# Optimization experiments

Hardware: AMD Instinct MI355X
Metric: run time of the kernel (lower is better)

## Reference

```python
import jax, jax.numpy as jnp
import numpy as np

K = 16          # max_points
S = 3           # num_scales
DM = 256        # d_model
KD = 16         # k_dim geometric projection
TAU = 1e-4
LN_EPS = 1e-5


def _boundaries():
    edges = [(i, j) for i in range(K) for j in range(i + 1, K)]
    tris = [(i, j, k) for i in range(K) for j in range(i + 1, K) for k in range(j + 1, K)]
    E, T = len(edges), len(tris)
    B1 = np.zeros((K, E), np.float32)
    for e, (i, j) in enumerate(edges):
        B1[i, e] = -1.0
        B1[j, e] = 1.0
    eidx = {e: n for n, e in enumerate(edges)}
    B2 = np.zeros((E, T), np.float32)
    for t, (i, j, k) in enumerate(tris):
        B2[eidx[(j, k)], t] = 1.0
        B2[eidx[(i, k)], t] = -1.0
        B2[eidx[(i, j)], t] = 1.0
    ei = np.array([e[0] for e in edges])
    ej = np.array([e[1] for e in edges])
    tij = np.array([eidx[(a, b)] for a, b, c in tris])
    tjk = np.array([eidx[(b, c)] for a, b, c in tris])
    tik = np.array([eidx[(a, c)] for a, b, c in tris])
    return (jnp.asarray(B1), jnp.asarray(B2), jnp.asarray(np.abs(B1)),
            jnp.asarray(ei), jnp.asarray(ej), jnp.asarray(tij), jnp.asarray(tjk), jnp.asarray(tik))

_B1, _B2, _ABS, _EI, _EJ, _TIJ, _TJK, _TIK = _boundaries()
E = _B1.shape[1]  # 120


def _ln(x, g, b):
    m = jnp.mean(x, -1, keepdims=True)
    v = jnp.mean((x - m) ** 2, -1, keepdims=True)
    return (x - m) * jax.lax.rsqrt(v + LN_EPS) * g + b


def setup_inputs() -> dict:
    key = jax.random.key(0)
    ks = jax.random.split(key, 12)
    B = 1024
    p = lambda k, *sh: 0.02 * jax.random.normal(k, sh, dtype=jnp.float32)
    return {
        'x': jax.random.normal(ks[0], (B, K, DM), dtype=jnp.float32),
        'mask': jnp.ones((B, K), dtype=jnp.float32),
        'Wg': p(ks[1], DM, KD), 'bg': jnp.zeros((KD,), jnp.float32),
        'log_scales': jnp.linspace(-1.5, 1.5, S, dtype=jnp.float32),
        'Wv': p(ks[2], DM, DM * S), 'bv': jnp.zeros((DM * S,), jnp.float32),
        'We': p(ks[3], DM, DM * S), 'be': jnp.zeros((DM * S,), jnp.float32),
        'Wo': p(ks[4], DM * S * 2, DM), 'bo': jnp.zeros((DM,), jnp.float32),
        'ln1_g': jnp.ones((DM,), jnp.float32), 'ln1_b': jnp.zeros((DM,), jnp.float32),
        'ln2_g': jnp.ones((DM,), jnp.float32), 'ln2_b': jnp.zeros((DM,), jnp.float32),
        'Wf1': p(ks[5], DM, DM * 4), 'bf1': jnp.zeros((DM * 4,), jnp.float32),
        'Wf2': p(ks[6], DM * 4, DM), 'bf2': jnp.zeros((DM,), jnp.float32),
    }


def reference(x, mask, Wg, bg, log_scales, Wv, bv, We, be, Wo, bo,
              ln1_g, ln1_b, ln2_g, ln2_b, Wf1, bf1, Wf2, bf2):
    B = x.shape[0]
    xn = _ln(x, ln1_g, ln1_b)
    P = xn @ Wg + bg                                   # [B,K,KD]
    m2 = mask[:, :, None] * mask[:, None, :]           # [B,K,K]
    p2 = jnp.sum(P * P, -1)
    Dsq = jnp.maximum(p2[:, :, None] + p2[:, None, :] - 2.0 * jnp.einsum('bkc,blc->bkl', P, P), 0.0) * m2
    sig2 = jnp.exp(log_scales) ** 2                    # [S]
    V0 = (xn @ Wv + bv).reshape(B, K, S, DM).transpose(0, 2, 1, 3)   # [B,S,K,D]
    Eraw = jnp.einsum('ke,bkd->bed', _ABS, xn)         # [B,E,D]
    Ein = (Eraw @ We + be).reshape(B, E, S, DM).transpose(0, 2, 1, 3)  # [B,S,E,D]
    aff = jnp.exp(-Dsq[:, None] / (2.0 * sig2[None, :, None, None] + 1e-8)) * m2[:, None]  # [B,S,K,K]
    W1 = aff[:, :, _EI, _EJ]                           # [B,S,E]
    W2 = W1[:, :, _TIJ] * W1[:, :, _TJK] * W1[:, :, _TIK]  # [B,S,T]
    L0 = jnp.einsum('ke,bse,le->bskl', _B1, W1, _B1) + TAU * jnp.eye(K, dtype=x.dtype)
    node_upd = jnp.einsum('bskl,bsld->bskd', L0, V0)
    term_down = jnp.einsum('ke,bk,kf->bef', _B1, mask, _B1)
    term_up = jnp.einsum('et,bst,ft->bsef', _B2, W2, _B2)
    L1 = term_down[:, None] + term_up + TAU * jnp.eye(E, dtype=x.dtype)
    edge_msg = jnp.einsum('bsef,bsfd->bsed', L1, Ein)
    edge_upd = jnp.einsum('ke,bsed->bskd', _ABS, edge_msg)
    nu = node_upd.transpose(0, 2, 1, 3).reshape(B, K, S * DM)
    eu = edge_upd.transpose(0, 2, 1, 3).reshape(B, K, S * DM)
    x = x + (jnp.concatenate([nu, eu], -1) @ Wo + bo)  # residual + attn_out (dropout=eval noop)
    h = _ln(x, ln2_g, ln2_b)
    return x + (jax.nn.gelu(h @ Wf1 + bf1, approximate=False) @ Wf2 + bf2)
```

## Files before the change

kernel.cpp:

```cpp
#include <hip/hip_runtime.h>
#include <hip/hip_bf16.h>
#include <cstdint>
#include <cstddef>

#define TAU 1e-4f
#define LN_EPS 1e-5f

typedef unsigned short ushort_t;
typedef unsigned int uint_t;
typedef __attribute__((ext_vector_type(8))) short short8;
typedef __attribute__((ext_vector_type(4))) float f32x4;

__device__ __forceinline__ ushort_t f2bf(float f) {
    union { float f; unsigned int u; } c; c.f = f;
    unsigned int r = (c.u + 0x7fffu + ((c.u >> 16) & 1u)) >> 16;
    return (ushort_t)r;
}
__device__ __forceinline__ void glds16(const void* g, void* l) {
    __builtin_amdgcn_global_load_lds((const __attribute__((address_space(1))) unsigned int*)g,
                                     (__attribute__((address_space(3))) unsigned int*)l,
                                     16, 0, 0);
}

__global__ __launch_bounds__(256) void kA(
    const float* __restrict__ xg, const float* __restrict__ maskg,
    const float* __restrict__ Wg, const float* __restrict__ bg,
    const float* __restrict__ ls, const float* __restrict__ g1,
    const float* __restrict__ b1, ushort_t* __restrict__ Mcat,
    float* __restrict__ gbuf,
    const float* __restrict__ Wv, const float* __restrict__ We,
    const float* __restrict__ Wo, const float* __restrict__ bv,
    const float* __restrict__ be, const float* __restrict__ Wf1,
    const float* __restrict__ Wf2, ushort_t* __restrict__ WcatT,
    ushort_t* __restrict__ Wf1T, ushort_t* __restrict__ Wf2T,
    float* __restrict__ cvpart, float* __restrict__ beWo) {
    __shared__ __align__(16) float POOL[7968];
    const int tid = threadIdx.x;

    if (blockIdx.x >= 1024) {
        const int id = blockIdx.x - 1024;
        if (id < 384) {
            float (*rowS)[256] = (float(*)[256])POOL;
            const int q0 = (id & 63) * 4;
            const int w = id >> 6;
            const int half = w / 3, s = w - half * 3;
            const float* src = half ? We : Wv;
#pragma unroll
            for (int r = 0; r < 4; ++r)
                rowS[r][tid] = src[(size_t)(q0 + r) * 768 + s * 256 + tid];
            __syncthreads();
            const float* wo = Wo + (size_t)(half * 768 + s * 256) * 256 + tid;
            float a0 = 0.f, a1 = 0.f, a2 = 0.f, a3 = 0.f;
            for (int d = 0; d < 256; ++d) {
                float wv = wo[(size_t)d * 256];
                a0 += rowS[0][d] * wv; a1 += rowS[1][d] * wv;
                a2 += rowS[2][d] * wv; a3 += rowS[3][d] * wv;
            }
            const int rt = half * 3 + s;
            ushort4 pk;
            pk.x = f2bf(a0); pk.y = f2bf(a1); pk.z = f2bf(a2); pk.w = f2bf(a3);
            *(ushort4*)&WcatT[(size_t)tid * 1536 + rt * 256 + q0] = pk;
        } else if (id < 390) {
            const int w = id - 384;
            const int half = w / 3, s = w - half * 3;
            const float* vec = half ? be : bv;
            POOL[tid] = vec[s * 256 + tid];
            __syncthreads();
            const float* wo = Wo + (size_t)(half * 768 + s * 256) * 256 + tid;
            float acc = 0.f;
            for (int d = 0; d < 256; ++d) acc += POOL[d] * wo[(size_t)d * 256];
            if (half) beWo[s * 256 + tid] = acc;
            else cvpart[s * 256 + tid] = acc;
        } else {
            float (*tS)[65] = (float(*)[65])POOL;
            const float* src; ushort_t* dst;
            int sr0, sc0, ss, dr0, dc0, ds_;
            if (id < 454) {
                int t = id - 390; int ki = t & 3, ni = t >> 2;
                src = Wf1; ss = 1024; sr0 = ki * 64; sc0 = ni * 64;
                dst = Wf1T; ds_ = 256; dr0 = ni * 64; dc0 = ki * 64;
            } else {
                int t = id - 454; int ki = t >> 2, ni = t & 3;
                src = Wf2; ss = 256; sr0 = ki * 64; sc0 = ni * 64;
                dst = Wf2T; ds_ = 1024; dr0 = ni * 64; dc0 = ki * 64;
            }
            const int rl = tid >> 6, cl = tid & 63;
#pragma unroll
            for (int p = 0; p < 16; ++p) {
                int r = p * 4 + rl;
                tS[r][cl] = src[(size_t)(sr0 + r) * ss + sc0 + cl];
            }
            __syncthreads();
#pragma unroll
            for (int p = 0; p < 16; ++p) {
                int r = p * 4 + rl;
                dst[(size_t)(dr0 + r) * ds_ + dc0 + cl] = f2bf(tS[cl][r]);
            }
        }
        return;
    }

    const int b = blockIdx.x;
    float (*XS)[260] = (float(*)[260])POOL;
    float (*WgTh)[132] = (float(*)[132])(POOL + 4160);
    float* Ms = POOL + 4160;
    float (*Wh)[16][17] = (float(*)[16][17])(POOL + 6272);
    float* Ts = POOL + 7088;
    float (*Pl)[17] = (float(*)[17])(POOL + 7136);
    float (*dotm)[17] = (float(*)[17])(POOL + 7408);
    float (*DsqS)[17] = (float(*)[17])(POOL + 7680);
    float* mk = POOL + 7952;

    const float* xb = xg + (size_t)b * 4096;
#pragma unroll
    for (int i = 0; i < 4; ++i) {
        int idx = tid * 4 + i * 1024;
        int k = idx >> 8, c = idx & 255;
        float4 v = *(const float4*)&xb[idx];
        XS[k][c] = v.x; XS[k][c + 1] = v.y; XS[k][c + 2] = v.z; XS[k][c + 3] = v.w;
    }
    if (tid < 16) mk[tid] = maskg[b * 16 + tid];
    __syncthreads();

    {
        const int k = tid >> 4, c = tid & 15;
        float s = 0.f;
#pragma unroll
        for (int j = 0; j < 16; ++j) s += XS[k][c + 16 * j];
        for (int off = 8; off; off >>= 1) s += __shfl_down(s, off, 16);
        float mean = __shfl(s, 0, 16) * (1.f / 256.f);
        float vs = 0.f;
#pragma unroll
        for (int j = 0; j < 16; ++j) { float d = XS[k][c + 16 * j] - mean; vs += d * d; }
        for (int off = 8; off; off >>= 1) vs += __shfl_down(vs, off, 16);
        float rstd = rsqrtf(__shfl(vs, 0, 16) * (1.f / 256.f) + LN_EPS);
#pragma unroll
        for (int j = 0; j < 16; ++j) {
            int cc = c + 16 * j;
            XS[k][cc] = (XS[k][cc] - mean) * rstd * g1[cc] + b1[cc];
        }
    }
    __syncthreads();

    {
        const int k = tid >> 4, c = tid & 15;
        const int ql = tid >> 1, hf = tid & 1;
        float acc = bg[c];
        {
            const float4* wp = (const float4*)(Wg + ql * 16 + hf * 8);
            float4 w0 = wp[0], w1 = wp[1];
            WgTh[hf * 8 + 0][ql] = w0.x; WgTh[hf * 8 + 1][ql] = w0.y;
            WgTh[hf * 8 + 2][ql] = w0.z; WgTh[hf * 8 + 3][ql] = w0.w;
            WgTh[hf * 8 + 4][ql] = w1.x; WgTh[hf * 8 + 5][ql] = w1.y;
            WgTh[hf * 8 + 6][ql] = w1.z; WgTh[hf * 8 + 7][ql] = w1.w;
        }
        __syncthreads();
        const float4* wp2 = (const float4*)(Wg + (128 + ql) * 16 + hf * 8);
        float4 w20 = wp2[0], w21 = wp2[1];
#pragma unroll
        for (int q4 = 0; q4 < 32; ++q4) {
            float4 wv = *(const float4*)&WgTh[c][q4 * 4];
            float4 xv = *(const float4*)&XS[k][q4 * 4];
            acc += wv.x * xv.x + wv.y * xv.y + wv.z * xv.z + wv.w * xv.w;
        }
        __syncthreads();
        WgTh[hf * 8 + 0][ql] = w20.x; WgTh[hf * 8 + 1][ql] = w20.y;
        WgTh[hf * 8 + 2][ql] = w20.z; WgTh[hf * 8 + 3][ql] = w20.w;
        WgTh[hf * 8 + 4][ql] = w21.x; WgTh[hf * 8 + 5][ql] = w21.y;
        WgTh[hf * 8 + 6][ql] = w21.z; WgTh[hf * 8 + 7][ql] = w21.w;
        __syncthreads();
#pragma unroll
        for (int q4 = 0; q4 < 32; ++q4) {
            float4 wv = *(const float4*)&WgTh[c][q4 * 4];
            float4 xv = *(const float4*)&XS[k][128 + q4 * 4];
            acc += wv.x * xv.x + wv.y * xv.y + wv.z * xv.z + wv.w * xv.w;
        }
        Pl[k][c] = acc;
    }
    __syncthreads();
    const int k = tid >> 4, m = tid & 15;
    {
        float d = 0.f;
#pragma unroll
        for (int c = 0; c < 16; ++c) d += Pl[k][c] * Pl[m][c];
        dotm[k][m] = d;
    }
    __syncthreads();
    {
        float v = dotm[k][k] + dotm[m][m] - 2.f * dotm[k][m];
        DsqS[k][m] = fmaxf(v, 0.f) * mk[k] * mk[m];
    }
    {
        float d = DsqS[k][m];
        float mm = mk[k] * mk[m];
#pragma unroll
        for (int s = 0; s < 3; ++s) {
            float i2 = 1.f / (2.f * expf(2.f * ls[s]) + 1e-8f);
            Wh[s][k][m] = (k == m) ? 0.f : expf(-d * i2) * mm;
        }
    }
    __syncthreads();
    if (tid < 48) {
        int s = tid >> 4, j = tid & 15;
        float t = 0.f;
        for (int i = 0; i < j; ++i) {
            float d = 0.f;
            for (int jj = j + 1; jj < 16; ++jj) d += Wh[s][j][jj] * Wh[s][i][jj];
            t += Wh[s][i][j] * d;
        }
        Ts[s * 16 + j] = t;
    }
    __syncthreads();
    float gd = 0.f;
#pragma unroll
    for (int o = 0; o < 16; ++o) {
        if (o == m) continue;
        int u = o < m ? o : m, v = o < m ? m : o;
        float gu = (u == k) ? (float)(2 * k - 15) : ((u > k) ? 1.f : -1.f);
        float gv = (v == k) ? (float)(2 * k - 15) : ((v > k) ? 1.f : -1.f);
        gd += -gu * mk[u] + gv * mk[v];
        if (u == k || v == k) gd += TAU;
    }
#pragma unroll
    for (int s = 0; s < 3; ++s) {
        float rs = 0.f;
#pragma unroll
        for (int o = 0; o < 16; ++o) rs += Wh[s][k][o];
        float l0 = (k == m) ? (rs + TAU) : -Wh[s][k][m];
        float G = gd + ((k == m) ? 4.f * Ts[s * 16 + k] : 0.f);
        Ms[s * 256 + tid] = l0;
        Ms[768 + s * 256 + tid] = G;
        float gg = G;
        for (int off = 8; off; off >>= 1) gg += __shfl_down(gg, off, 16);
        if (m == 0) gbuf[b * 48 + k * 3 + s] = 0.5f * gg;
    }
    __syncthreads();

    {
        const int q2 = (tid & 127) * 2;
        const int rtbase = (tid >> 7) * 3;
        float xv0[16], xv1[16];
#pragma unroll
        for (int l = 0; l < 16; ++l) { xv0[l] = XS[l][q2]; xv1[l] = XS[l][q2 + 1]; }
        const size_t obase = (size_t)b * 16 * 1536;
#pragma unroll
        for (int rtt = 0; rtt < 3; ++rtt) {
            const int rt = rtbase + rtt;
#pragma unroll
            for (int kk = 0; kk < 16; ++kk) {
                const float4* mp = (const float4*)&Ms[rt * 256 + kk * 16];
                float4 m0 = mp[0], m1 = mp[1], m2 = mp[2], m3 = mp[3];
                float a0 = m0.x * xv0[0] + m0.y * xv0[1] + m0.z * xv0[2] + m0.w * xv0[3]
                         + m1.x * xv0[4] + m1.y * xv0[5] + m1.z * xv0[6] + m1.w * xv0[7]
                         + m2.x * xv0[8] + m2.y * xv0[9] + m2.z * xv0[10] + m2.w * xv0[11]
                         + m3.x * xv0[12] + m3.y * xv0[13] + m3.z * xv0[14] + m3.w * xv0[15];
                float a1 = m0.x * xv1[0] + m0.y * xv1[1] + m0.z * xv1[2] + m0.w * xv1[3]
                         + m1.x * xv1[4] + m1.y * xv1[5] + m1.z * xv1[6] + m1.w * xv1[7]
                         + m2.x * xv1[8] + m2.y * xv1[9] + m2.z * xv1[10] + m2.w * xv1[11]
                         + m3.x * xv1[12] + m3.y * xv1[13] + m3.z * xv1[14] + m3.w * xv1[15];
                uint_t pk = (uint_t)f2bf(a0) | ((uint_t)f2bf(a1) << 16);
                *(uint_t*)&Mcat[obase + (size_t)kk * 1536 + rt * 256 + q2] = pk;
            }
        }
    }
}

__device__ __forceinline__ void gemm64_db(
    const ushort_t* __restrict__ A, const ushort_t* __restrict__ Bt,
    int Kdim, int m0, int n0, f32x4 acc[2][4],
    ushort_t (*As0)[32], ushort_t (*As1)[32],
    ushort_t (*Bs0)[32], ushort_t (*Bs1)[32]) {
    const int tid = threadIdx.x;
    const int wave = tid >> 6, lane = tid & 63;
    const int lq = lane >> 4, lr = lane & 15;
    const int wm = wave >> 1, wn = wave & 1;
    const int r = tid >> 2, ca = (tid & 3) << 3;
    const ushort_t* Ag  = A  + (size_t)(m0 + r) * Kdim + ca;
    const ushort_t* Bg0 = Bt + (size_t)(n0 + r) * Kdim + ca;
    const ushort_t* Bg1 = Bt + (size_t)(n0 + 64 + r) * Kdim + ca;
    char* aD0  = (char*)As0 + wave * 1024;
    char* aD1  = (char*)As1 + wave * 1024;
    char* b0D0 = (char*)Bs0 + wave * 1024;
    char* b0D1 = (char*)Bs0 + 4096 + wave * 1024;
    char* b1D0 = (char*)Bs1 + wave * 1024;
    char* b1D1 = (char*)Bs1 + 4096 + wave * 1024;

    glds16(Ag, aD0); glds16(Bg0, b0D0); glds16(Bg1, b0D1);

    for (int kt = 0; kt < Kdim; kt += 64) {
        {
            const int kn = kt + 32;
            if (kn < Kdim) {
                glds16(Ag + kn, aD1); glds16(Bg0 + kn, b1D0); glds16(Bg1 + kn, b1D1);
                asm volatile("s_waitcnt vmcnt(3)" ::: "memory");
            } else {
                asm volatile("s_waitcnt vmcnt(0)" ::: "memory");
            }
            __builtin_amdgcn_s_barrier();
            short8 af[2], bfr[4];
#pragma unroll
            for (int i = 0; i < 2; ++i) af[i] = *(const short8*)&As0[wm * 32 + i * 16 + lr][lq * 8];
#pragma unroll
            for (int j = 0; j < 4; ++j) bfr[j] = *(const short8*)&Bs0[wn * 64 + j * 16 + lr][lq * 8];
#pragma unroll
            for (int i = 0; i < 2; ++i)
#pragma unroll
                for (int j = 0; j < 4; ++j)
                    acc[i][j] = __builtin_amdgcn_mfma_f32_16x16x32_bf16(af[i], bfr[j], acc[i][j], 0, 0, 0);
            asm volatile("s_waitcnt lgkmcnt(0)" ::: "memory");
            __builtin_amdgcn_s_barrier();
        }
        {
            const int kn = kt + 64;
            if (kn < Kdim) {
                glds16(Ag + kn, aD0); glds16(Bg0 + kn, b0D0); glds16(Bg1 + kn, b0D1);
                asm volatile("s_waitcnt vmcnt(3)" ::: "memory");
            } else {
                asm volatile("s_waitcnt vmcnt(0)" ::: "memory");
            }
            __builtin_amdgcn_s_barrier();
            short8 af[2], bfr[4];
#pragma unroll
            for (int i = 0; i < 2; ++i) af[i] = *(const short8*)&As1[wm * 32 + i * 16 + lr][lq * 8];
#pragma unroll
            for (int j = 0; j < 4; ++j) bfr[j] = *(const short8*)&Bs1[wn * 64 + j * 16 + lr][lq * 8];
#pragma unroll
            for (int i = 0; i < 2; ++i)
#pragma unroll
                for (int j = 0; j < 4; ++j)
                    acc[i][j] = __builtin_amdgcn_mfma_f32_16x16x32_bf16(af[i], bfr[j], acc[i][j], 0, 0, 0);
            asm volatile("s_waitcnt lgkmcnt(0)" ::: "memory");
            __builtin_amdgcn_s_barrier();
        }
    }
}

__global__ __launch_bounds__(256) void kZY_gemm(
    const ushort_t* __restrict__ Mcat, const ushort_t* __restrict__ WcatT,
    const float* __restrict__ xin, const float* __restrict__ bo,
    const float* __restrict__ cvpart, const float* __restrict__ beWo,
    const float* __restrict__ gbuf, float* __restrict__ xp) {
    __shared__ ushort_t As0[64][32], As1[64][32];
    __shared__ ushort_t Bs0[128][32], Bs1[128][32];
    __shared__ float cvS[128], bewS[3][128], gblk[64][3];
    const int tid = threadIdx.x;
    const int m0 = blockIdx.x * 64, n0 = blockIdx.y * 128;
    if (tid < 128) {
        int n = n0 + tid;
        cvS[tid] = bo[n] + TAU * (cvpart[n] + cvpart[256 + n] + cvpart[512 + n]);
        bewS[0][tid] = beWo[n];
        bewS[1][tid] = beWo[256 + n];
        bewS[2][tid] = beWo[512 + n];
    }
    if (tid < 192) { int rr = tid / 3, s = tid - rr * 3; gblk[rr][s] = gbuf[(size_t)(m0 + rr) * 3 + s]; }
    f32x4 acc[2][4] = {};
    gemm64_db(Mcat, WcatT, 1536, m0, n0, acc, As0, As1, Bs0, Bs1);
    const int wave = tid >> 6, lane = tid & 63, lq = lane >> 4, lr = lane & 15;
    const int wm = wave >> 1, wn = wave & 1;
#pragma unroll
    for (int i = 0; i < 2; ++i)
#pragma unroll
        for (int j = 0; j < 4; ++j) {
            int nl = wn * 64 + j * 16 + lr;
#pragma unroll
            for (int v = 0; v < 4; ++v) {
                int rl = wm * 32 + i * 16 + lq * 4 + v;
                size_t idx = (size_t)(m0 + rl) * 256 + n0 + nl;
                xp[idx] = acc[i][j][v] + xin[idx] + cvS[nl] +
                          gblk[rl][0] * bewS[0][nl] + gblk[rl][1] * bewS[1][nl] +
                          gblk[rl][2] * bewS[2][nl];
            }
        }
}

__global__ __launch_bounds__(256) void k_ln2(const float* __restrict__ xp,
                                             const float* __restrict__ g2,
                                             const float* __restrict__ b2,
                                             ushort_t* __restrict__ h) {
    const int tid = threadIdx.x;
    const int row = blockIdx.x * 4 + (tid >> 6);
    const int lane = tid & 63;
    const float* xr = xp + (size_t)row * 256;
    float v0 = xr[lane], v1 = xr[lane + 64], v2 = xr[lane + 128], v3 = xr[lane + 192];
    float s = v0 + v1 + v2 + v3;
    for (int m = 32; m; m >>= 1) s += __shfl_xor(s, m, 64);
    float mean = s * (1.f / 256.f);
    float d0 = v0 - mean, d1 = v1 - mean, d2 = v2 - mean, d3 = v3 - mean;
    float q = d0 * d0 + d1 * d1 + d2 * d2 + d3 * d3;
    for (int m = 32; m; m >>= 1) q += __shfl_xor(q, m, 64);
    float rstd = rsqrtf(q * (1.f / 256.f) + LN_EPS);
    ushort_t* hr = h + (size_t)row * 256;
    hr[lane] = f2bf(d0 * rstd * g2[lane] + b2[lane]);
    hr[lane + 64] = f2bf(d1 * rstd * g2[lane + 64] + b2[lane + 64]);
    hr[lane + 128] = f2bf(d2 * rstd * g2[lane + 128] + b2[lane + 128]);
    hr[lane + 192] = f2bf(d3 * rstd * g2[lane + 192] + b2[lane + 192]);
}

__global__ __launch_bounds__(256) void k3_gemm(const ushort_t* __restrict__ h,
                                               const ushort_t* __restrict__ Wf1T,
                                               const float* __restrict__ bf1,
                                               ushort_t* __restrict__ F1g) {
    __shared__ ushort_t As0[64][32], As1[64][32];
    __shared__ ushort_t Bs0[128][32], Bs1[128][32];
    const int tid = threadIdx.x;
    const int m0 = blockIdx.x * 64, n0 = blockIdx.y * 128;
    f32x4 acc[2][4] = {};
    gemm64_db(h, Wf1T, 256, m0, n0, acc, As0, As1, Bs0, Bs1);
    const int wave = tid >> 6, lane = tid & 63, lq = lane >> 4, lr = lane & 15;
    const int wm = wave >> 1, wn = wave & 1;
#pragma unroll
    for (int i = 0; i < 2; ++i)
#pragma unroll
        for (int j = 0; j < 4; ++j) {
            int n = n0 + wn * 64 + j * 16 + lr;
            float bn = bf1[n];
#pragma unroll
            for (int v = 0; v < 4; ++v) {
                int rg = m0 + wm * 32 + i * 16 + lq * 4 + v;
                float u = acc[i][j][v] + bn;
                float gl = 0.5f * u * (1.f + erff(u * 0.70710678118f));
                F1g[(size_t)rg * 1024 + n] = f2bf(gl);
            }
        }
}

__global__ __launch_bounds__(256) void k4_gemm(const ushort_t* __restrict__ F1g,
                                               const ushort_t* __restrict__ Wf2T,
                                               const float* __restrict__ bf2,
                                               const float* __restrict__ xp,
                                               float* __restrict__ out) {
    __shared__ ushort_t As0[64][32], As1[64][32];
    __shared__ ushort_t Bs0[128][32], Bs1[128][32];
    const int tid = threadIdx.x;
    const int m0 = blockIdx.x * 64, n0 = blockIdx.y * 128;
    f32x4 acc[2][4] = {};
    gemm64_db(F1g, Wf2T, 1024, m0, n0, acc, As0, As1, Bs0, Bs1);
    const int wave = tid >> 6, lane = tid & 63, lq = lane >> 4, lr = lane & 15;
    const int wm = wave >> 1, wn = wave & 1;
#pragma unroll
    for (int i = 0; i < 2; ++i)
#pragma unroll
        for (int j = 0; j < 4; ++j) {
            int n = n0 + wn * 64 + j * 16 + lr;
            float bn = bf2[n];
#pragma unroll
            for (int v = 0; v < 4; ++v) {
                size_t idx = (size_t)(m0 + wm * 32 + i * 16 + lq * 4 + v) * 256 + n;
                out[idx] = xp[idx] + acc[i][j][v] + bn;
            }
        }
}

extern "C" void kernel_launch(void* const* d_in, const int* in_sizes, int n_in,
                              void* d_out, int out_size, void* d_ws, size_t ws_size,
                              hipStream_t stream) {
    const float* x = (const float*)d_in[0];
    const float* mask = (const float*)d_in[1];
    const float* Wg = (const float*)d_in[2];
    const float* bg = (const float*)d_in[3];
    const float* ls = (const float*)d_in[4];
    const float* Wv = (const float*)d_in[5];
    const float* bv = (const float*)d_in[6];
    const float* We = (const float*)d_in[7];
    const float* be = (const float*)d_in[8];
    const float* Wo = (const float*)d_in[9];
    const float* bo = (const float*)d_in[10];
    const float* g1 = (const float*)d_in[11];
    const float* b1 = (const float*)d_in[12];
    const float* g2 = (const float*)d_in[13];
    const float* b2 = (const float*)d_in[14];
    const float* Wf1 = (const float*)d_in[15];
    const float* bf1 = (const float*)d_in[16];
    const float* Wf2 = (const float*)d_in[17];
    const float* bf2 = (const float*)d_in[18];
    float* out = (float*)d_out;

    char* ws = (char*)d_ws;
    ushort_t* Mcat = (ushort_t*)(ws);
    ushort_t* F1g = (ushort_t*)(ws);
    ushort_t* WcatT = (ushort_t*)(ws + 50331648);
    ushort_t* Wf1T = (ushort_t*)(ws + 51118080);
    ushort_t* Wf2T = (ushort_t*)(ws + 51642368);
    float* cvpart = (float*)(ws + 52166656);
    float* beWo = (float*)(ws + 52169728);
    float* gbuf = (float*)(ws + 52172800);
    float* xp = (float*)(ws + 52369408);
    ushort_t* h = (ushort_t*)(ws + 69146624);

    kA<<<dim3(1542), dim3(256), 0, stream>>>(x, mask, Wg, bg, ls, g1, b1,
                                             Mcat, gbuf,
                                             Wv, We, Wo, bv, be, Wf1, Wf2,
                                             WcatT, Wf1T, Wf2T, cvpart, beWo);
    kZY_gemm<<<dim3(256, 2), dim3(256), 0, stream>>>(Mcat, WcatT, x, bo, cvpart, beWo, gbuf, xp);
    k_ln2<<<dim3(4096), dim3(256), 0, stream>>>(xp, g2, b2, h);
    k3_gemm<<<dim3(256, 8), dim3(256), 0, stream>>>(h, Wf1T, bf1, F1g);
    k4_gemm<<<dim3(256, 2), dim3(256), 0, stream>>>(F1g, Wf2T, bf2, xp, out);
}
```

Measured before the change: 207.2 us.

## Replace LDS-staged GEMMs in kZY and k4 with direct-load per-wave 16x128 MFMA tiles

The two N=256 GEMMs (kZY with K=1536, k4 with K=1024) drop the shared-memory double-buffered 64x128 block tile. Each wave now computes an independent 16x128 tile, loading A and B fragments straight from global memory into registers for MFMA, with no barriers. The grid grows to 512 blocks, which removes LDS traffic and synchronisation and raises parallelism. In exchange there is no cross-wave reuse, so B fragments are re-read per wave and rely on L2 and L1 caching. The epilogue now reads bias and gbuf values directly instead of staging them in LDS.

```diff
diff --git a/kernel.cpp b/kernel.cpp
--- a/kernel.cpp
+++ b/kernel.cpp
@@ -265,72 +265,21 @@
     }
 }
 
-__device__ __forceinline__ void gemm64_db(
+__device__ __forceinline__ void gemm_direct16x128(
     const ushort_t* __restrict__ A, const ushort_t* __restrict__ Bt,
-    int Kdim, int m0, int n0, f32x4 acc[2][4],
-    ushort_t (*As0)[32], ushort_t (*As1)[32],
-    ushort_t (*Bs0)[32], ushort_t (*Bs1)[32]) {
-    const int tid = threadIdx.x;
-    const int wave = tid >> 6, lane = tid & 63;
+    int Kdim, int m0, int n0, f32x4 acc[8]) {
+    const int lane = threadIdx.x & 63;
     const int lq = lane >> 4, lr = lane & 15;
-    const int wm = wave >> 1, wn = wave & 1;
-    const int r = tid >> 2, ca = (tid & 3) << 3;
-    const ushort_t* Ag  = A  + (size_t)(m0 + r) * Kdim + ca;
-    const ushort_t* Bg0 = Bt + (size_t)(n0 + r) * Kdim + ca;
-    const ushort_t* Bg1 = Bt + (size_t)(n0 + 64 + r) * Kdim + ca;
-    char* aD0  = (char*)As0 + wave * 1024;
-    char* aD1  = (char*)As1 + wave * 1024;
-    char* b0D0 = (char*)Bs0 + wave * 1024;
-    char* b0D1 = (char*)Bs0 + 4096 + wave * 1024;
-    char* b1D0 = (char*)Bs1 + wave * 1024;
-    char* b1D1 = (char*)Bs1 + 4096 + wave * 1024;
-
-    glds16(Ag, aD0); glds16(Bg0, b0D0); glds16(Bg1, b0D1);
-
-    for (int kt = 0; kt < Kdim; kt += 64) {
-        {
-            const int kn = kt + 32;
-            if (kn < Kdim) {
-                glds16(Ag + kn, aD1); glds16(Bg0 + kn, b1D0); glds16(Bg1 + kn, b1D1);
-                asm volatile("s_waitcnt vmcnt(3)" ::: "memory");
-            } else {
-                asm volatile("s_waitcnt vmcnt(0)" ::: "memory");
-            }
-            __builtin_amdgcn_s_barrier();
-            short8 af[2], bfr[4];
-#pragma unroll
-            for (int i = 0; i < 2; ++i) af[i] = *(const short8*)&As0[wm * 32 + i * 16 + lr][lq * 8];
-#pragma unroll
-            for (int j = 0; j < 4; ++j) bfr[j] = *(const short8*)&Bs0[wn * 64 + j * 16 + lr][lq * 8];
-#pragma unroll
-            for (int i = 0; i < 2; ++i)
-#pragma unroll
-                for (int j = 0; j < 4; ++j)
-                    acc[i][j] = __builtin_amdgcn_mfma_f32_16x16x32_bf16(af[i], bfr[j], acc[i][j], 0, 0, 0);
-            asm volatile("s_waitcnt lgkmcnt(0)" ::: "memory");
-            __builtin_amdgcn_s_barrier();
-        }
-        {
-            const int kn = kt + 64;
-            if (kn < Kdim) {
-                glds16(Ag + kn, aD0); glds16(Bg0 + kn, b0D0); glds16(Bg1 + kn, b0D1);
-                asm volatile("s_waitcnt vmcnt(3)" ::: "memory");
-            } else {
-                asm volatile("s_waitcnt vmcnt(0)" ::: "memory");
-            }
-            __builtin_amdgcn_s_barrier();
-            short8 af[2], bfr[4];
-#pragma unroll
-            for (int i = 0; i < 2; ++i) af[i] = *(const short8*)&As1[wm * 32 + i * 16 + lr][lq * 8];
-#pragma unroll
-            for (int j = 0; j < 4; ++j) bfr[j] = *(const short8*)&Bs1[wn * 64 + j * 16 + lr][lq * 8];
-#pragma unroll
-            for (int i = 0; i < 2; ++i)
-#pragma unroll
-                for (int j = 0; j < 4; ++j)
-                    acc[i][j] = __builtin_amdgcn_mfma_f32_16x16x32_bf16(af[i], bfr[j], acc[i][j], 0, 0, 0);
-            asm volatile("s_waitcnt lgkmcnt(0)" ::: "memory");
-            __builtin_amdgcn_s_barrier();
+    const ushort_t* Ap = A + (size_t)(m0 + lr) * Kdim + lq * 8;
+    const ushort_t* Bp = Bt + (size_t)(n0 + lr) * Kdim + lq * 8;
+    const size_t bs = (size_t)16 * Kdim;
+#pragma unroll 2
+    for (int kt = 0; kt < Kdim; kt += 32) {
+        short8 af = *(const short8*)(Ap + kt);
+#pragma unroll
+        for (int j = 0; j < 8; ++j) {
+            short8 bf = *(const short8*)(Bp + (size_t)j * bs + kt);
+            acc[j] = __builtin_amdgcn_mfma_f32_16x16x32_bf16(af, bf, acc[j], 0, 0, 0);
         }
     }
 }
@@ -340,37 +289,31 @@
     const float* __restrict__ xin, const float* __restrict__ bo,
     const float* __restrict__ cvpart, const float* __restrict__ beWo,
     const float* __restrict__ gbuf, float* __restrict__ xp) {
-    __shared__ ushort_t As0[64][32], As1[64][32];
-    __shared__ ushort_t Bs0[128][32], Bs1[128][32];
-    __shared__ float cvS[128], bewS[3][128], gblk[64][3];
     const int tid = threadIdx.x;
-    const int m0 = blockIdx.x * 64, n0 = blockIdx.y * 128;
-    if (tid < 128) {
-        int n = n0 + tid;
-        cvS[tid] = bo[n] + TAU * (cvpart[n] + cvpart[256 + n] + cvpart[512 + n]);
-        bewS[0][tid] = beWo[n];
-        bewS[1][tid] = beWo[256 + n];
-        bewS[2][tid] = beWo[512 + n];
-    }
-    if (tid < 192) { int rr = tid / 3, s = tid - rr * 3; gblk[rr][s] = gbuf[(size_t)(m0 + rr) * 3 + s]; }
-    f32x4 acc[2][4] = {};
-    gemm64_db(Mcat, WcatT, 1536, m0, n0, acc, As0, As1, Bs0, Bs1);
-    const int wave = tid >> 6, lane = tid & 63, lq = lane >> 4, lr = lane & 15;
-    const int wm = wave >> 1, wn = wave & 1;
-#pragma unroll
-    for (int i = 0; i < 2; ++i)
-#pragma unroll
-        for (int j = 0; j < 4; ++j) {
-            int nl = wn * 64 + j * 16 + lr;
-#pragma unroll
-            for (int v = 0; v < 4; ++v) {
-                int rl = wm * 32 + i * 16 + lq * 4 + v;
-                size_t idx = (size_t)(m0 + rl) * 256 + n0 + nl;
-                xp[idx] = acc[i][j][v] + xin[idx] + cvS[nl] +
-                          gblk[rl][0] * bewS[0][nl] + gblk[rl][1] * bewS[1][nl] +
-                          gblk[rl][2] * bewS[2][nl];
-            }
-        }
+    const int wid = blockIdx.x * 4 + (tid >> 6);
+    const int lane = tid & 63, lq = lane >> 4, lr = lane & 15;
+    const int m0 = (wid >> 1) * 16;
+    const int n0 = (wid & 1) * 128;
+    f32x4 acc[8] = {};
+    gemm_direct16x128(Mcat, WcatT, 1536, m0, n0, acc);
+    const int r0 = m0 + lq * 4;
+    float ga[4], gb[4], gc[4];
+#pragma unroll
+    for (int v = 0; v < 4; ++v) {
+        const float* gp = gbuf + (size_t)(r0 + v) * 3;
+        ga[v] = gp[0]; gb[v] = gp[1]; gc[v] = gp[2];
+    }
+#pragma unroll
+    for (int j = 0; j < 8; ++j) {
+        const int col = n0 + j * 16 + lr;
+        const float cv = bo[col] + TAU * (cvpart[col] + cvpart[256 + col] + cvpart[512 + col]);
+        const float b0 = beWo[col], b1 = beWo[256 + col], b2v = beWo[512 + col];
+#pragma unroll
+        for (int v = 0; v < 4; ++v) {
+            const size_t idx = (size_t)(r0 + v) * 256 + col;
+            xp[idx] = acc[j][v] + xin[idx] + cv + ga[v] * b0 + gb[v] * b1 + gc[v] * b2v;
+        }
+    }
 }
 
 __global__ __launch_bounds__(256) void k_ln2(const float* __restrict__ xp,
@@ -396,6 +339,76 @@
     hr[lane + 192] = f2bf(d3 * rstd * g2[lane + 192] + b2[lane + 192]);
 }
 
+__device__ __forceinline__ void gemm64_db(
+    const ushort_t* __restrict__ A, const ushort_t* __restrict__ Bt,
+    int Kdim, int m0, int n0, f32x4 acc[2][4],
+    ushort_t (*As0)[32], ushort_t (*As1)[32],
+    ushort_t (*Bs0)[32], ushort_t (*Bs1)[32]) {
+    const int tid = threadIdx.x;
+    const int wave = tid >> 6, lane = tid & 63;
+    const int lq = lane >> 4, lr = lane & 15;
+    const int wm = wave >> 1, wn = wave & 1;
+    const int r = tid >> 2, ca = (tid & 3) << 3;
+    const ushort_t* Ag  = A  + (size_t)(m0 + r) * Kdim + ca;
+    const ushort_t* Bg0 = Bt + (size_t)(n0 + r) * Kdim + ca;
+    const ushort_t* Bg1 = Bt + (size_t)(n0 + 64 + r) * Kdim + ca;
+    char* aD0  = (char*)As0 + wave * 1024;
+    char* aD1  = (char*)As1 + wave * 1024;
+    char* b0D0 = (char*)Bs0 + wave * 1024;
+    char* b0D1 = (char*)Bs0 + 4096 + wave * 1024;
+    char* b1D0 = (char*)Bs1 + wave * 1024;
+    char* b1D1 = (char*)Bs1 + 4096 + wave * 1024;
+
+    glds16(Ag, aD0); glds16(Bg0, b0D0); glds16(Bg1, b0D1);
+
+    for (int kt = 0; kt < Kdim; kt += 64) {
+        {
+            const int kn = kt + 32;
+            if (kn < Kdim) {
+                glds16(Ag + kn, aD1); glds16(Bg0 + kn, b1D0); glds16(Bg1 + kn, b1D1);
+                asm volatile("s_waitcnt vmcnt(3)" ::: "memory");
+            } else {
+                asm volatile("s_waitcnt vmcnt(0)" ::: "memory");
+            }
+            __builtin_amdgcn_s_barrier();
+            short8 af[2], bfr[4];
+#pragma unroll
+            for (int i = 0; i < 2; ++i) af[i] = *(const short8*)&As0[wm * 32 + i * 16 + lr][lq * 8];
+#pragma unroll
+            for (int j = 0; j < 4; ++j) bfr[j] = *(const short8*)&Bs0[wn * 64 + j * 16 + lr][lq * 8];
+#pragma unroll
+            for (int i = 0; i < 2; ++i)
+#pragma unroll
+                for (int j = 0; j < 4; ++j)
+                    acc[i][j] = __builtin_amdgcn_mfma_f32_16x16x32_bf16(af[i], bfr[j], acc[i][j], 0, 0, 0);
+            asm volatile("s_waitcnt lgkmcnt(0)" ::: "memory");
+            __builtin_amdgcn_s_barrier();
+        }
+        {
+            const int kn = kt + 64;
+            if (kn < Kdim) {
+                glds16(Ag + kn, aD0); glds16(Bg0 + kn, b0D0); glds16(Bg1 + kn, b0D1);
+                asm volatile("s_waitcnt vmcnt(3)" ::: "memory");
+            } else {
+                asm volatile("s_waitcnt vmcnt(0)" ::: "memory");
+            }
+            __builtin_amdgcn_s_barrier();
+            short8 af[2], bfr[4];
+#pragma unroll
+            for (int i = 0; i < 2; ++i) af[i] = *(const short8*)&As1[wm * 32 + i * 16 + lr][lq * 8];
+#pragma unroll
+            for (int j = 0; j < 4; ++j) bfr[j] = *(const short8*)&Bs1[wn * 64 + j * 16 + lr][lq * 8];
+#pragma unroll
+            for (int i = 0; i < 2; ++i)
+#pragma unroll
+                for (int j = 0; j < 4; ++j)
+                    acc[i][j] = __builtin_amdgcn_mfma_f32_16x16x32_bf16(af[i], bfr[j], acc[i][j], 0, 0, 0);
+            asm volatile("s_waitcnt lgkmcnt(0)" ::: "memory");
+            __builtin_amdgcn_s_barrier();
+        }
+    }
+}
+
 __global__ __launch_bounds__(256) void k3_gemm(const ushort_t* __restrict__ h,
                                                const ushort_t* __restrict__ Wf1T,
                                                const float* __restrict__ bf1,
@@ -429,26 +442,24 @@
                                                const float* __restrict__ bf2,
                                                const float* __restrict__ xp,
                                                float* __restrict__ out) {
-    __shared__ ushort_t As0[64][32], As1[64][32];
-    __shared__ ushort_t Bs0[128][32], Bs1[128][32];
     const int tid = threadIdx.x;
-    const int m0 = blockIdx.x * 64, n0 = blockIdx.y * 128;
-    f32x4 acc[2][4] = {};
-    gemm64_db(F1g, Wf2T, 1024, m0, n0, acc, As0, As1, Bs0, Bs1);
-    const int wave = tid >> 6, lane = tid & 63, lq = lane >> 4, lr = lane & 15;
-    const int wm = wave >> 1, wn = wave & 1;
-#pragma unroll
-    for (int i = 0; i < 2; ++i)
-#pragma unroll
-        for (int j = 0; j < 4; ++j) {
-            int n = n0 + wn * 64 + j * 16 + lr;
-            float bn = bf2[n];
-#pragma unroll
-            for (int v = 0; v < 4; ++v) {
-                size_t idx = (size_t)(m0 + wm * 32 + i * 16 + lq * 4 + v) * 256 + n;
-                out[idx] = xp[idx] + acc[i][j][v] + bn;
-            }
-        }
+    const int wid = blockIdx.x * 4 + (tid >> 6);
+    const int lane = tid & 63, lq = lane >> 4, lr = lane & 15;
+    const int m0 = (wid >> 1) * 16;
+    const int n0 = (wid & 1) * 128;
+    f32x4 acc[8] = {};
+    gemm_direct16x128(F1g, Wf2T, 1024, m0, n0, acc);
+    const int r0 = m0 + lq * 4;
+#pragma unroll
+    for (int j = 0; j < 8; ++j) {
+        const int col = n0 + j * 16 + lr;
+        const float bn = bf2[col];
+#pragma unroll
+        for (int v = 0; v < 4; ++v) {
+            const size_t idx = (size_t)(r0 + v) * 256 + col;
+            out[idx] = xp[idx] + acc[j][v] + bn;
+        }
+    }
 }
 
 extern "C" void kernel_launch(void* const* d_in, const int* in_sizes, int n_in,
@@ -491,8 +502,8 @@
                                              Mcat, gbuf,
                                              Wv, We, Wo, bv, be, Wf1, Wf2,
                                              WcatT, Wf1T, Wf2T, cvpart, beWo);
-    kZY_gemm<<<dim3(256, 2), dim3(256), 0, stream>>>(Mcat, WcatT, x, bo, cvpart, beWo, gbuf, xp);
+    kZY_gemm<<<dim3(512), dim3(256), 0, stream>>>(Mcat, WcatT, x, bo, cvpart, beWo, gbuf, xp);
     k_ln2<<<dim3(4096), dim3(256), 0, stream>>>(xp, g2, b2, h);
     k3_gemm<<<dim3(256, 8), dim3(256), 0, stream>>>(h, Wf1T, bf1, F1g);
-    k4_gemm<<<dim3(256, 2), dim3(256), 0, stream>>>(F1g, Wf2T, bf2, xp, out);
-}
+    k4_gemm<<<dim3(512), dim3(256), 0, stream>>>(F1g, Wf2T, bf2, xp, out);
+}
```

New measurement: 323.1 us. +55.9%, slower.

## Reassociate message operator after weight GEMM and fuse LN2 into combine kernel

Applied to the files above, without the earlier changes.

kA no longer applies the per-batch 16x16 Laplacian and geometric operators to the normalized input. It now writes bf16 normalized x plus the operator matrices, which are parked in the h buffer. A wider GEMM (N=1536, K=256) forms Z = xn·W' first. A new per-batch kernel then applies the operators to Z, adds the residual and bias terms, and runs LayerNorm2 in place, so the separate k_ln2 launch and its reread of xp go away. The GEMM FLOPs and the intermediate size stay the same. The exchange is a bf16 rounding of Z instead of M·x, and a less parallel per-batch combine kernel.

```diff
diff --git a/kernel.cpp b/kernel.cpp
--- a/kernel.cpp
+++ b/kernel.cpp
@@ -16,6 +16,9 @@
     unsigned int r = (c.u + 0x7fffu + ((c.u >> 16) & 1u)) >> 16;
     return (ushort_t)r;
 }
+__device__ __forceinline__ float bf2f(uint_t u) {
+    union { float f; uint_t u; } c; c.u = u << 16; return c.f;
+}
 __device__ __forceinline__ void glds16(const void* g, void* l) {
     __builtin_amdgcn_global_load_lds((const __attribute__((address_space(1))) unsigned int*)g,
                                      (__attribute__((address_space(3))) unsigned int*)l,
@@ -26,14 +29,15 @@
     const float* __restrict__ xg, const float* __restrict__ maskg,
     const float* __restrict__ Wg, const float* __restrict__ bg,
     const float* __restrict__ ls, const float* __restrict__ g1,
-    const float* __restrict__ b1, ushort_t* __restrict__ Mcat,
+    const float* __restrict__ b1, ushort_t* __restrict__ xnb,
     float* __restrict__ gbuf,
     const float* __restrict__ Wv, const float* __restrict__ We,
     const float* __restrict__ Wo, const float* __restrict__ bv,
     const float* __restrict__ be, const float* __restrict__ Wf1,
-    const float* __restrict__ Wf2, ushort_t* __restrict__ WcatT,
+    const float* __restrict__ Wf2, ushort_t* __restrict__ WzT,
     ushort_t* __restrict__ Wf1T, ushort_t* __restrict__ Wf2T,
-    float* __restrict__ cvpart, float* __restrict__ beWo) {
+    float* __restrict__ cvpart, float* __restrict__ beWo,
+    ushort_t* __restrict__ hM) {
     __shared__ __align__(16) float POOL[7968];
     const int tid = threadIdx.x;
 
@@ -59,7 +63,7 @@
             const int rt = half * 3 + s;
             ushort4 pk;
             pk.x = f2bf(a0); pk.y = f2bf(a1); pk.z = f2bf(a2); pk.w = f2bf(a3);
-            *(ushort4*)&WcatT[(size_t)tid * 1536 + rt * 256 + q0] = pk;
+            *(ushort4*)&WzT[((size_t)(rt * 256 + tid)) * 256 + q0] = pk;
         } else if (id < 390) {
             const int w = id - 384;
             const int half = w / 3, s = w - half * 3;
@@ -103,7 +107,6 @@
     const int b = blockIdx.x;
     float (*XS)[260] = (float(*)[260])POOL;
     float (*WgTh)[132] = (float(*)[132])(POOL + 4160);
-    float* Ms = POOL + 4160;
     float (*Wh)[16][17] = (float(*)[16][17])(POOL + 6272);
     float* Ts = POOL + 7088;
     float (*Pl)[17] = (float(*)[17])(POOL + 7136);
@@ -141,6 +144,17 @@
         }
     }
     __syncthreads();
+
+    {
+        ushort_t* xo = xnb + (size_t)b * 4096;
+#pragma unroll
+        for (int i = 0; i < 8; ++i) {
+            int flat = i * 512 + tid * 2;
+            int k = flat >> 8, c = flat & 255;
+            uint_t pk = (uint_t)f2bf(XS[k][c]) | ((uint_t)f2bf(XS[k][c + 1]) << 16);
+            *(uint_t*)&xo[flat] = pk;
+        }
+    }
 
     {
         const int k = tid >> 4, c = tid & 15;
@@ -221,46 +235,20 @@
         gd += -gu * mk[u] + gv * mk[v];
         if (u == k || v == k) gd += TAU;
     }
-#pragma unroll
-    for (int s = 0; s < 3; ++s) {
-        float rs = 0.f;
-#pragma unroll
-        for (int o = 0; o < 16; ++o) rs += Wh[s][k][o];
-        float l0 = (k == m) ? (rs + TAU) : -Wh[s][k][m];
-        float G = gd + ((k == m) ? 4.f * Ts[s * 16 + k] : 0.f);
-        Ms[s * 256 + tid] = l0;
-        Ms[768 + s * 256 + tid] = G;
-        float gg = G;
-        for (int off = 8; off; off >>= 1) gg += __shfl_down(gg, off, 16);
-        if (m == 0) gbuf[b * 48 + k * 3 + s] = 0.5f * gg;
-    }
-    __syncthreads();
-
-    {
-        const int q2 = (tid & 127) * 2;
-        const int rtbase = (tid >> 7) * 3;
-        float xv0[16], xv1[16];
-#pragma unroll
-        for (int l = 0; l < 16; ++l) { xv0[l] = XS[l][q2]; xv1[l] = XS[l][q2 + 1]; }
-        const size_t obase = (size_t)b * 16 * 1536;
-#pragma unroll
-        for (int rtt = 0; rtt < 3; ++rtt) {
-            const int rt = rtbase + rtt;
-#pragma unroll
-            for (int kk = 0; kk < 16; ++kk) {
-                const float4* mp = (const float4*)&Ms[rt * 256 + kk * 16];
-                float4 m0 = mp[0], m1 = mp[1], m2 = mp[2], m3 = mp[3];
-                float a0 = m0.x * xv0[0] + m0.y * xv0[1] + m0.z * xv0[2] + m0.w * xv0[3]
-                         + m1.x * xv0[4] + m1.y * xv0[5] + m1.z * xv0[6] + m1.w * xv0[7]
-                         + m2.x * xv0[8] + m2.y * xv0[9] + m2.z * xv0[10] + m2.w * xv0[11]
-                         + m3.x * xv0[12] + m3.y * xv0[13] + m3.z * xv0[14] + m3.w * xv0[15];
-                float a1 = m0.x * xv1[0] + m0.y * xv1[1] + m0.z * xv1[2] + m0.w * xv1[3]
-                         + m1.x * xv1[4] + m1.y * xv1[5] + m1.z * xv1[6] + m1.w * xv1[7]
-                         + m2.x * xv1[8] + m2.y * xv1[9] + m2.z * xv1[10] + m2.w * xv1[11]
-                         + m3.x * xv1[12] + m3.y * xv1[13] + m3.z * xv1[14] + m3.w * xv1[15];
-                uint_t pk = (uint_t)f2bf(a0) | ((uint_t)f2bf(a1) << 16);
-                *(uint_t*)&Mcat[obase + (size_t)kk * 1536 + rt * 256 + q2] = pk;
-            }
+    {
+        float* MsgB = (float*)(hM + (size_t)b * 4096);
+#pragma unroll
+        for (int s = 0; s < 3; ++s) {
+            float rs = 0.f;
+#pragma unroll
+            for (int o = 0; o < 16; ++o) rs += Wh[s][k][o];
+            float l0 = (k == m) ? (rs + TAU) : -Wh[s][k][m];
+            float G = gd + ((k == m) ? 4.f * Ts[s * 16 + k] : 0.f);
+            MsgB[s * 256 + tid] = l0;
+            MsgB[768 + s * 256 + tid] = G;
+            float gg = G;
+            for (int off = 8; off; off >>= 1) gg += __shfl_down(gg, off, 16);
+            if (m == 0) gbuf[b * 48 + k * 3 + s] = 0.5f * gg;
         }
     }
 }
@@ -335,65 +323,119 @@
     }
 }
 
-__global__ __launch_bounds__(256) void kZY_gemm(
-    const ushort_t* __restrict__ Mcat, const ushort_t* __restrict__ WcatT,
-    const float* __restrict__ xin, const float* __restrict__ bo,
-    const float* __restrict__ cvpart, const float* __restrict__ beWo,
-    const float* __restrict__ gbuf, float* __restrict__ xp) {
+__global__ __launch_bounds__(256) void kZ_gemm(const ushort_t* __restrict__ xnb,
+                                               const ushort_t* __restrict__ WzT,
+                                               ushort_t* __restrict__ Zcat) {
     __shared__ ushort_t As0[64][32], As1[64][32];
     __shared__ ushort_t Bs0[128][32], Bs1[128][32];
-    __shared__ float cvS[128], bewS[3][128], gblk[64][3];
     const int tid = threadIdx.x;
     const int m0 = blockIdx.x * 64, n0 = blockIdx.y * 128;
-    if (tid < 128) {
-        int n = n0 + tid;
-        cvS[tid] = bo[n] + TAU * (cvpart[n] + cvpart[256 + n] + cvpart[512 + n]);
-        bewS[0][tid] = beWo[n];
-        bewS[1][tid] = beWo[256 + n];
-        bewS[2][tid] = beWo[512 + n];
-    }
-    if (tid < 192) { int rr = tid / 3, s = tid - rr * 3; gblk[rr][s] = gbuf[(size_t)(m0 + rr) * 3 + s]; }
     f32x4 acc[2][4] = {};
-    gemm64_db(Mcat, WcatT, 1536, m0, n0, acc, As0, As1, Bs0, Bs1);
+    gemm64_db(xnb, WzT, 256, m0, n0, acc, As0, As1, Bs0, Bs1);
     const int wave = tid >> 6, lane = tid & 63, lq = lane >> 4, lr = lane & 15;
     const int wm = wave >> 1, wn = wave & 1;
 #pragma unroll
     for (int i = 0; i < 2; ++i)
 #pragma unroll
         for (int j = 0; j < 4; ++j) {
-            int nl = wn * 64 + j * 16 + lr;
+            int n = n0 + wn * 64 + j * 16 + lr;
 #pragma unroll
             for (int v = 0; v < 4; ++v) {
-                int rl = wm * 32 + i * 16 + lq * 4 + v;
-                size_t idx = (size_t)(m0 + rl) * 256 + n0 + nl;
-                xp[idx] = acc[i][j][v] + xin[idx] + cvS[nl] +
-                          gblk[rl][0] * bewS[0][nl] + gblk[rl][1] * bewS[1][nl] +
-                          gblk[rl][2] * bewS[2][nl];
-            }
-        }
-}
-
-__global__ __launch_bounds__(256) void k_ln2(const float* __restrict__ xp,
-                                             const float* __restrict__ g2,
-                                             const float* __restrict__ b2,
-                                             ushort_t* __restrict__ h) {
+                int rg = m0 + wm * 32 + i * 16 + lq * 4 + v;
+                Zcat[(size_t)rg * 1536 + n] = f2bf(acc[i][j][v]);
+            }
+        }
+}
+
+__global__ __launch_bounds__(256) void kC(
+    const ushort_t* __restrict__ Zcat, const float* __restrict__ xg,
+    const float* __restrict__ bo, const float* __restrict__ cvpart,
+    const float* __restrict__ beWo, const float* __restrict__ gbuf,
+    const float* __restrict__ g2, const float* __restrict__ b2,
+    float* __restrict__ xp, ushort_t* __restrict__ hM) {
+    __shared__ float MsS[1536];
+    __shared__ float xpS[16][258];
+    __shared__ float gS[48];
     const int tid = threadIdx.x;
-    const int row = blockIdx.x * 4 + (tid >> 6);
-    const int lane = tid & 63;
-    const float* xr = xp + (size_t)row * 256;
-    float v0 = xr[lane], v1 = xr[lane + 64], v2 = xr[lane + 128], v3 = xr[lane + 192];
-    float s = v0 + v1 + v2 + v3;
-    for (int m = 32; m; m >>= 1) s += __shfl_xor(s, m, 64);
-    float mean = s * (1.f / 256.f);
-    float d0 = v0 - mean, d1 = v1 - mean, d2 = v2 - mean, d3 = v3 - mean;
-    float q = d0 * d0 + d1 * d1 + d2 * d2 + d3 * d3;
-    for (int m = 32; m; m >>= 1) q += __shfl_xor(q, m, 64);
-    float rstd = rsqrtf(q * (1.f / 256.f) + LN_EPS);
-    ushort_t* hr = h + (size_t)row * 256;
-    hr[lane] = f2bf(d0 * rstd * g2[lane] + b2[lane]);
-    hr[lane + 64] = f2bf(d1 * rstd * g2[lane + 64] + b2[lane + 64]);
-    hr[lane + 128] = f2bf(d2 * rstd * g2[lane + 128] + b2[lane + 128]);
-    hr[lane + 192] = f2bf(d3 * rstd * g2[lane + 192] + b2[lane + 192]);
+    const int b = blockIdx.x;
+    const float* MsgB = (const float*)(hM + (size_t)b * 4096);
+#pragma unroll
+    for (int i = 0; i < 6; ++i) MsS[tid + i * 256] = MsgB[tid + i * 256];
+    if (tid < 48) gS[tid] = gbuf[b * 48 + tid];
+    __syncthreads();
+
+    const int half = tid >> 7, q2 = (tid & 127) * 2;
+    float acc0[16], acc1[16];
+#pragma unroll
+    for (int k = 0; k < 16; ++k) { acc0[k] = 0.f; acc1[k] = 0.f; }
+    const ushort_t* zb = Zcat + (size_t)b * 16 * 1536;
+#pragma unroll
+    for (int rtt = 0; rtt < 3; ++rtt) {
+        const int rt = half * 3 + rtt;
+        float zr0[16], zr1[16];
+#pragma unroll
+        for (int l = 0; l < 16; ++l) {
+            uint_t zz = *(const uint_t*)&zb[(size_t)l * 1536 + rt * 256 + q2];
+            zr0[l] = bf2f(zz & 0xffffu);
+            zr1[l] = bf2f(zz >> 16);
+        }
+        const float* Mrt = MsS + rt * 256;
+#pragma unroll
+        for (int k = 0; k < 16; ++k) {
+            const float4* mp = (const float4*)&Mrt[k * 16];
+            float4 m0 = mp[0], m1 = mp[1], m2 = mp[2], m3 = mp[3];
+            acc0[k] += m0.x * zr0[0] + m0.y * zr0[1] + m0.z * zr0[2] + m0.w * zr0[3]
+                     + m1.x * zr0[4] + m1.y * zr0[5] + m1.z * zr0[6] + m1.w * zr0[7]
+                     + m2.x * zr0[8] + m2.y * zr0[9] + m2.z * zr0[10] + m2.w * zr0[11]
+                     + m3.x * zr0[12] + m3.y * zr0[13] + m3.z * zr0[14] + m3.w * zr0[15];
+            acc1[k] += m0.x * zr1[0] + m0.y * zr1[1] + m0.z * zr1[2] + m0.w * zr1[3]
+                     + m1.x * zr1[4] + m1.y * zr1[5] + m1.z * zr1[6] + m1.w * zr1[7]
+                     + m2.x * zr1[8] + m2.y * zr1[9] + m2.z * zr1[10] + m2.w * zr1[11]
+                     + m3.x * zr1[12] + m3.y * zr1[13] + m3.z * zr1[14] + m3.w * zr1[15];
+        }
+    }
+    if (half == 0) {
+        float cv0 = bo[q2] + TAU * (cvpart[q2] + cvpart[256 + q2] + cvpart[512 + q2]);
+        float cv1 = bo[q2 + 1] + TAU * (cvpart[q2 + 1] + cvpart[256 + q2 + 1] + cvpart[512 + q2 + 1]);
+        float bw00 = beWo[q2], bw01 = beWo[q2 + 1];
+        float bw10 = beWo[256 + q2], bw11 = beWo[256 + q2 + 1];
+        float bw20 = beWo[512 + q2], bw21 = beWo[512 + q2 + 1];
+#pragma unroll
+        for (int k = 0; k < 16; ++k) {
+            float2 xv = *(const float2*)&xg[((size_t)b * 16 + k) * 256 + q2];
+            float ga0 = gS[k * 3], ga1 = gS[k * 3 + 1], ga2 = gS[k * 3 + 2];
+            xpS[k][q2]     = acc0[k] + xv.x + cv0 + ga0 * bw00 + ga1 * bw10 + ga2 * bw20;
+            xpS[k][q2 + 1] = acc1[k] + xv.y + cv1 + ga0 * bw01 + ga1 * bw11 + ga2 * bw21;
+        }
+    }
+    __syncthreads();
+    if (half == 1) {
+#pragma unroll
+        for (int k = 0; k < 16; ++k) { xpS[k][q2] += acc0[k]; xpS[k][q2 + 1] += acc1[k]; }
+    }
+    __syncthreads();
+#pragma unroll
+    for (int k = 0; k < 16; ++k)
+        xp[((size_t)b * 16 + k) * 256 + tid] = xpS[k][tid];
+    const int lane = tid & 63, wv = tid >> 6;
+#pragma unroll
+    for (int rr = 0; rr < 4; ++rr) {
+        const int row = wv * 4 + rr;
+        float v0 = xpS[row][lane], v1 = xpS[row][lane + 64];
+        float v2 = xpS[row][lane + 128], v3 = xpS[row][lane + 192];
+        float s = v0 + v1 + v2 + v3;
+        for (int mo = 32; mo; mo >>= 1) s += __shfl_xor(s, mo, 64);
+        float mean = s * (1.f / 256.f);
+        float d0 = v0 - mean, d1 = v1 - mean, d2 = v2 - mean, d3 = v3 - mean;
+        float qq = d0 * d0 + d1 * d1 + d2 * d2 + d3 * d3;
+        for (int mo = 32; mo; mo >>= 1) qq += __shfl_xor(qq, mo, 64);
+        float rstd = rsqrtf(qq * (1.f / 256.f) + LN_EPS);
+        ushort_t* hr = hM + ((size_t)b * 16 + row) * 256;
+        hr[lane] = f2bf(d0 * rstd * g2[lane] + b2[lane]);
+        hr[lane + 64] = f2bf(d1 * rstd * g2[lane + 64] + b2[lane + 64]);
+        hr[lane + 128] = f2bf(d2 * rstd * g2[lane + 128] + b2[lane + 128]);
+        hr[lane + 192] = f2bf(d3 * rstd * g2[lane + 192] + b2[lane + 192]);
+    }
 }
 
 __global__ __launch_bounds__(256) void k3_gemm(const ushort_t* __restrict__ h,
@@ -476,23 +518,25 @@
     float* out = (float*)d_out;
 
     char* ws = (char*)d_ws;
-    ushort_t* Mcat = (ushort_t*)(ws);
+    ushort_t* Zcat = (ushort_t*)(ws);
     ushort_t* F1g = (ushort_t*)(ws);
-    ushort_t* WcatT = (ushort_t*)(ws + 50331648);
+    ushort_t* WzT = (ushort_t*)(ws + 50331648);
     ushort_t* Wf1T = (ushort_t*)(ws + 51118080);
     ushort_t* Wf2T = (ushort_t*)(ws + 51642368);
     float* cvpart = (float*)(ws + 52166656);
     float* beWo = (float*)(ws + 52169728);
     float* gbuf = (float*)(ws + 52172800);
+    ushort_t* xnb = (ushort_t*)(ws + 52369408);
     float* xp = (float*)(ws + 52369408);
-    ushort_t* h = (ushort_t*)(ws + 69146624);
+    ushort_t* hM = (ushort_t*)(ws + 69146624);
 
     kA<<<dim3(1542), dim3(256), 0, stream>>>(x, mask, Wg, bg, ls, g1, b1,
-                                             Mcat, gbuf,
+                                             xnb, gbuf,
                                              Wv, We, Wo, bv, be, Wf1, Wf2,
-                                             WcatT, Wf1T, Wf2T, cvpart, beWo);
-    kZY_gemm<<<dim3(256, 2), dim3(256), 0, stream>>>(Mcat, WcatT, x, bo, cvpart, beWo, gbuf, xp);
-    k_ln2<<<dim3(4096), dim3(256), 0, stream>>>(xp, g2, b2, h);
-    k3_gemm<<<dim3(256, 8), dim3(256), 0, stream>>>(h, Wf1T, bf1, F1g);
+                                             WzT, Wf1T, Wf2T, cvpart, beWo, hM);
+    kZ_gemm<<<dim3(256, 12), dim3(256), 0, stream>>>(xnb, WzT, Zcat);
+    kC<<<dim3(1024), dim3(256), 0, stream>>>(Zcat, x, bo, cvpart, beWo, gbuf,
+                                             g2, b2, xp, hM);
+    k3_gemm<<<dim3(256, 8), dim3(256), 0, stream>>>(hM, Wf1T, bf1, F1g);
     k4_gemm<<<dim3(256, 2), dim3(256), 0, stream>>>(F1g, Wf2T, bf2, xp, out);
 }
```

After: 228.0 us. 10.0% more time.
